# Kernel tuning notes

Measured on AMD Instinct MI355X. Metric: run time of the kernel, lower is better.

The kernel has to match this reference:

```python
import jax, jax.numpy as jnp
import numpy as np

BATCH, SEQ, IN, HID, OUT = 128, 1024, 256, 512, 256


def setup_inputs() -> dict:
    key = jax.random.key(0)
    k_x, k_wi, k_bi, k_wo, k_bo = jax.random.split(key, 5)
    # torch.nn.Linear default init: U(-1/sqrt(fan_in), 1/sqrt(fan_in))
    s_i = 1.0 / np.sqrt(IN + HID)
    s_o = 1.0 / np.sqrt(HID)
    return {
        "x": jax.random.normal(k_x, (BATCH, SEQ, IN), dtype=jnp.float32),
        "W_i2h": jax.random.uniform(k_wi, (HID, IN + HID), jnp.float32, -s_i, s_i),
        "b_i2h": jax.random.uniform(k_bi, (HID,), jnp.float32, -s_i, s_i),
        "W_h2o": jax.random.uniform(k_wo, (OUT, HID), jnp.float32, -s_o, s_o),
        "b_h2o": jax.random.uniform(k_bo, (OUT,), jnp.float32, -s_o, s_o),
    }


def reference(x, W_i2h, b_i2h, W_h2o, b_h2o):
    batch = x.shape[0]
    hid = W_i2h.shape[0]
    # Split i2h weight into input and hidden blocks: cat(x_t, h) @ W.T == x_t @ Wx.T + h @ Wh.T
    Wx = W_i2h[:, : x.shape[-1]]  # (hid, in)
    Wh = W_i2h[:, x.shape[-1] :]  # (hid, hid)
    # Precompute input contributions for all timesteps in one GEMM: (B,S,hid)
    xW = jnp.einsum("bsi,hi->bsh", x, Wx) + b_i2h

    def step(h, xw_t):
        h_new = jnp.tanh(xw_t + h @ Wh.T)
        return h_new, h_new

    h0 = jnp.zeros((batch, hid), dtype=x.dtype)
    h_last, hs = jax.lax.scan(step, h0, jnp.swapaxes(xW, 0, 1))  # hs: (S,B,hid)
    hs = jnp.swapaxes(hs, 0, 1)  # (B,S,hid)
    outputs = jnp.einsum("bsh,oh->bso", hs, W_h2o) + b_h2o  # (B,S,out)
    return outputs, h_last
```

## Files before the change

### kernel.cpp

```cpp
#include <hip/hip_runtime.h>

typedef __attribute__((ext_vector_type(8))) short bf16frag;
typedef __attribute__((ext_vector_type(4))) float f32x4;

constexpr int B = 128, S = 1024, DI = 256, DH = 512, DO = 256;
constexpr int NBUF = 4;
constexpr size_t OUT_MAIN = (size_t)B * S * DO;
constexpr size_t HBUF_BYTES = (size_t)NBUF * B * DH * 2;
constexpr size_t FLAGS_BYTES = 8 * 64 * 4;
constexpr int WH_OFF = 0;
constexpr int WX_OFF = 16384;
constexpr int WHO_OFF = 24576;
constexpr int LDS_BYTES = 65536;

__device__ __forceinline__ void release_vm() {
  asm volatile("s_waitcnt vmcnt(0)" ::: "memory");
}
__device__ __forceinline__ void acquire_cc() {
  asm volatile("" ::: "memory");
}

__device__ __forceinline__ unsigned short f2bf(float f) {
  unsigned int u = __float_as_uint(f);
  u += 0x7fffu + ((u >> 16) & 1u);
  return (unsigned short)(u >> 16);
}
__device__ __forceinline__ float bf2f(unsigned short h) {
  return __uint_as_float(((unsigned int)h) << 16);
}
__device__ __forceinline__ float fast_tanh(float x) {
  float e = __expf(2.0f * x);
  return 1.0f - 2.0f * __builtin_amdgcn_rcpf(e + 1.0f);
}
__device__ __forceinline__ bf16frag cvt8(float4 a, float4 b) {
  bf16frag r;
  r[0]=(short)f2bf(a.x); r[1]=(short)f2bf(a.y); r[2]=(short)f2bf(a.z); r[3]=(short)f2bf(a.w);
  r[4]=(short)f2bf(b.x); r[5]=(short)f2bf(b.y); r[6]=(short)f2bf(b.z); r[7]=(short)f2bf(b.w);
  return r;
}
__device__ __forceinline__ bf16frag load8(const void* base, size_t off, bool fp32m) {
  if (fp32m) {
    const float4* p = reinterpret_cast<const float4*>((const float*)base + off);
    return cvt8(p[0], p[1]);
  }
  return *reinterpret_cast<const bf16frag*>((const unsigned short*)base + off);
}

__device__ __forceinline__ void cluster_wait(const int* f01, const int* f2, int T1, int T2) {
  const int lane = threadIdx.x & 63;
  const int* addr;
  int thr;
  if (lane < 32)      { addr = f01 + lane;        thr = T1; }
  else if (lane < 48) { addr = f2 + (lane - 32);  thr = T2; }
  else                { addr = f01;               thr = (int)0x80000000; }
  int guard = 0;
  while (true) {
    int v = __hip_atomic_load(addr, __ATOMIC_RELAXED, __HIP_MEMORY_SCOPE_AGENT);
    if (__all(v >= thr)) break;
    if (++guard > (1 << 26)) break;
    __builtin_amdgcn_s_sleep(1);
  }
}

__global__ void __launch_bounds__(192, 1)
rnn_persistent(const void* __restrict__ xv,
               const void* __restrict__ Wi2hv,
               const void* __restrict__ biv,
               const void* __restrict__ Whov,
               const void* __restrict__ bov,
               void* __restrict__ outv,
               unsigned short* __restrict__ hbuf,
               int* __restrict__ flags) {
  extern __shared__ unsigned short lds[];
  const int tid = threadIdx.x;
  const int lane = tid & 63;
  const int wave = tid >> 6;
  const int blk = blockIdx.x;
  const int c   = blk & 7;
  const int mem = blk >> 3;
  const int b0  = c * 16;
  const int n_base = mem * 32;
  const int o_base = mem * 16;

  bool fp32m;
  {
    const unsigned short* xu = (const unsigned short*)xv;
    int c0 = 0;
    for (int i = lane; i < 4096; i += 64)
      c0 += (((xu[i] >> 7) & 0xFF) >= 0xC0);
    #pragma unroll
    for (int s = 32; s; s >>= 1) c0 += __shfl_xor(c0, s, 64);
    fp32m = (c0 > 100);
  }

  for (int i = tid; i < 32 * 64; i += 192) {
    int r = i >> 6, bk = i & 63;
    bf16frag v = load8(Wi2hv, (size_t)(n_base + r) * 768 + 256 + bk * 8, fp32m);
    *reinterpret_cast<bf16frag*>(lds + WH_OFF + r * 512 + ((bk ^ (r & 7)) * 8)) = v;
  }
  for (int i = tid; i < 32 * 32; i += 192) {
    int r = i >> 5, bk = i & 31;
    bf16frag v = load8(Wi2hv, (size_t)(n_base + r) * 768 + bk * 8, fp32m);
    *reinterpret_cast<bf16frag*>(lds + WX_OFF + r * 256 + ((bk ^ (r & 7)) * 8)) = v;
  }
  for (int i = tid; i < 16 * 64; i += 192) {
    int r = i >> 6, bk = i & 63;
    bf16frag v = load8(Whov, (size_t)(o_base + r) * 512 + bk * 8, fp32m);
    *reinterpret_cast<bf16frag*>(lds + WHO_OFF + r * 512 + ((bk ^ (r & 7)) * 8)) = v;
  }
  __syncthreads();

  int* f01 = flags + c * 64;
  int* f2  = f01 + 32;
  const int q  = lane >> 4;
  const int ln = lane & 15;
  float* outf = (float*)outv;
  unsigned short* outh = (unsigned short*)outv;

  if (wave < 2) {
    const int nlB  = wave * 16 + ln;
    const int n_g  = n_base + nlB;
    const float bias = fp32m ? ((const float*)biv)[n_g]
                             : bf2f(((const unsigned short*)biv)[n_g]);
    const int swz = nlB & 7;
    const size_t xrow = (size_t)(b0 + ln) * (S * DI) + q * 8;
    const int flag_idx = mem * 2 + wave;
    const size_t hrow_off = (size_t)(b0 + ln) * DH + q * 8;

    bf16frag xf[8];
    #pragma unroll
    for (int cc = 0; cc < 8; ++cc)
      xf[cc] = load8(xv, xrow + cc * 32, fp32m);

    for (int t = 0; t < S; ++t) {
      f32x4 acc = {bias, bias, bias, bias};
      #pragma unroll
      for (int cc = 0; cc < 8; ++cc) {
        bf16frag wf = *reinterpret_cast<const bf16frag*>(
            lds + WX_OFF + nlB * 256 + (((cc * 4 + q) ^ swz) * 8));
        acc = __builtin_amdgcn_mfma_f32_16x16x32_bf16(xf[cc], wf, acc, 0, 0, 0);
      }
      if (t + 1 < S) {
        #pragma unroll
        for (int cc = 0; cc < 8; ++cc)
          xf[cc] = load8(xv, xrow + (size_t)(t + 1) * DI + cc * 32, fp32m);
      }
      if (t > 0) {
        cluster_wait(f01, f2, t, t - 3);
        acquire_cc();
        const unsigned short* hsrc = hbuf + (size_t)((t - 1) & 3) * (B * DH) + hrow_off;
        unsigned long long hlo[16], hhi[16];
        #pragma unroll
        for (int cc = 0; cc < 16; ++cc) {
          const unsigned long long* p = reinterpret_cast<const unsigned long long*>(hsrc + cc * 32);
          hlo[cc] = __hip_atomic_load(p,     __ATOMIC_RELAXED, __HIP_MEMORY_SCOPE_AGENT);
          hhi[cc] = __hip_atomic_load(p + 1, __ATOMIC_RELAXED, __HIP_MEMORY_SCOPE_AGENT);
        }
        #pragma unroll
        for (int cc = 0; cc < 16; ++cc) {
          union { unsigned long long u[2]; bf16frag f; } cvt;
          cvt.u[0] = hlo[cc]; cvt.u[1] = hhi[cc];
          bf16frag wf = *reinterpret_cast<const bf16frag*>(
              lds + WH_OFF + nlB * 512 + (((cc * 4 + q) ^ swz) * 8));
          acc = __builtin_amdgcn_mfma_f32_16x16x32_bf16(cvt.f, wf, acc, 0, 0, 0);
        }
      }
      unsigned short* hdst = hbuf + (size_t)(t & 3) * (B * DH);
      #pragma unroll
      for (int r = 0; r < 4; ++r) {
        float hv = fast_tanh(acc[r]);
        unsigned short hu = f2bf(hv);
        unsigned int other = __shfl_xor((unsigned int)hu, 1, 64);
        if ((lane & 1) == 0) {
          unsigned int packed = (unsigned int)hu | (other << 16);
          __hip_atomic_store(reinterpret_cast<unsigned int*>(
              hdst + (size_t)(b0 + q * 4 + r) * DH + n_g),
              packed, __ATOMIC_RELAXED, __HIP_MEMORY_SCOPE_AGENT);
        }
        if (t == S - 1) {
          size_t hidx = OUT_MAIN + (size_t)(b0 + q * 4 + r) * DH + n_g;
          if (fp32m) outf[hidx] = hv; else outh[hidx] = hu;
        }
      }
      release_vm();
      if (lane == 0)
        __hip_atomic_store(f01 + flag_idx, t + 1, __ATOMIC_RELAXED, __HIP_MEMORY_SCOPE_AGENT);
    }
  } else {
    const int o_g = o_base + ln;
    const float bias = fp32m ? ((const float*)bov)[o_g]
                             : bf2f(((const unsigned short*)bov)[o_g]);
    const int swz = ln & 7;
    const size_t hrow_off = (size_t)(b0 + ln) * DH + q * 8;
    for (int u = 0; u < S; ++u) {
      cluster_wait(f01, f2, u + 1, (int)0x80000000);
      acquire_cc();
      const unsigned short* hsrc = hbuf + (size_t)(u & 3) * (B * DH) + hrow_off;
      unsigned long long hlo[16], hhi[16];
      #pragma unroll
      for (int cc = 0; cc < 16; ++cc) {
        const unsigned long long* p = reinterpret_cast<const unsigned long long*>(hsrc + cc * 32);
        hlo[cc] = __hip_atomic_load(p,     __ATOMIC_RELAXED, __HIP_MEMORY_SCOPE_AGENT);
        hhi[cc] = __hip_atomic_load(p + 1, __ATOMIC_RELAXED, __HIP_MEMORY_SCOPE_AGENT);
      }
      f32x4 acc = {bias, bias, bias, bias};
      #pragma unroll
      for (int cc = 0; cc < 16; ++cc) {
        union { unsigned long long u[2]; bf16frag f; } cvt;
        cvt.u[0] = hlo[cc]; cvt.u[1] = hhi[cc];
        bf16frag wf = *reinterpret_cast<const bf16frag*>(
            lds + WHO_OFF + ln * 512 + (((cc * 4 + q) ^ swz) * 8));
        acc = __builtin_amdgcn_mfma_f32_16x16x32_bf16(cvt.f, wf, acc, 0, 0, 0);
      }
      #pragma unroll
      for (int r = 0; r < 4; ++r) {
        size_t oidx = ((size_t)(b0 + q * 4 + r) * S + u) * DO + o_g;
        if (fp32m) outf[oidx] = acc[r]; else outh[oidx] = f2bf(acc[r]);
      }
      release_vm();
      if (lane == 0)
        __hip_atomic_store(f2 + mem, u + 1, __ATOMIC_RELAXED, __HIP_MEMORY_SCOPE_AGENT);
    }
  }
}

extern "C" void kernel_launch(void* const* d_in, const int* in_sizes, int n_in,
                              void* d_out, int out_size, void* d_ws, size_t ws_size,
                              hipStream_t stream) {
  const void* x    = d_in[0];
  const void* Wi2h = d_in[1];
  const void* bi   = d_in[2];
  const void* Who  = d_in[3];
  const void* bo   = d_in[4];
  void* out = d_out;
  unsigned short* hbuf = (unsigned short*)d_ws;
  int* flags = (int*)((char*)d_ws + HBUF_BYTES);
  if (ws_size < HBUF_BYTES + FLAGS_BYTES) return;

  hipMemsetAsync(flags, 0, FLAGS_BYTES, stream);

  void* args[] = { (void*)&x, (void*)&Wi2h, (void*)&bi, (void*)&Who, (void*)&bo,
                   (void*)&out, (void*)&hbuf, (void*)&flags };
  hipError_t e = hipLaunchCooperativeKernel((void*)rnn_persistent, dim3(128), dim3(192),
                                            args, LDS_BYTES, stream);
  if (e != hipSuccess) {
    rnn_persistent<<<dim3(128), dim3(192), LDS_BYTES, stream>>>(
        x, Wi2h, bi, Who, bo, out, hbuf, flags);
  }
}
```

Before: 8.605 ms.

## Replace per-block flag polling with per-slot atomic counters and deeper h ring buffer

Each wave used to poll 48 per-block flags with a wave-wide vote. Now it waits on two per-slot atomic counters that producers increment with fetch_add, so the wait reads only two addresses. The h ring buffer grows from 4 to up to 16 slots, sized to the workspace, which lets the output-projection waves lag further behind the recurrence before they stall it. The cost is contended atomic increments on a shared counter from 32 or 16 blocks per step, plus more workspace memory.

Measured after the change: 8.835 ms. 2.7% more time.

```diff
diff --git a/kernel.cpp b/kernel.cpp
--- a/kernel.cpp
+++ b/kernel.cpp
@@ -4,10 +4,10 @@
 typedef __attribute__((ext_vector_type(4))) float f32x4;
 
 constexpr int B = 128, S = 1024, DI = 256, DH = 512, DO = 256;
-constexpr int NBUF = 4;
+constexpr int MAXNB = 16;
 constexpr size_t OUT_MAIN = (size_t)B * S * DO;
-constexpr size_t HBUF_BYTES = (size_t)NBUF * B * DH * 2;
-constexpr size_t FLAGS_BYTES = 8 * 64 * 4;
+constexpr size_t SLOT_BYTES = (size_t)B * DH * 2;
+constexpr size_t FLAGS_BYTES = 8 * 2 * MAXNB * 64;
 constexpr int WH_OFF = 0;
 constexpr int WX_OFF = 16384;
 constexpr int WHO_OFF = 24576;
@@ -46,17 +46,12 @@
   return *reinterpret_cast<const bf16frag*>((const unsigned short*)base + off);
 }
 
-__device__ __forceinline__ void cluster_wait(const int* f01, const int* f2, int T1, int T2) {
-  const int lane = threadIdx.x & 63;
-  const int* addr;
-  int thr;
-  if (lane < 32)      { addr = f01 + lane;        thr = T1; }
-  else if (lane < 48) { addr = f2 + (lane - 32);  thr = T2; }
-  else                { addr = f01;               thr = (int)0x80000000; }
+__device__ __forceinline__ void wait2(const int* a1, int t1, const int* a2, int t2) {
   int guard = 0;
   while (true) {
-    int v = __hip_atomic_load(addr, __ATOMIC_RELAXED, __HIP_MEMORY_SCOPE_AGENT);
-    if (__all(v >= thr)) break;
+    int v1 = __hip_atomic_load(a1, __ATOMIC_RELAXED, __HIP_MEMORY_SCOPE_AGENT);
+    int v2 = __hip_atomic_load(a2, __ATOMIC_RELAXED, __HIP_MEMORY_SCOPE_AGENT);
+    if (v1 >= t1 && v2 >= t2) break;
     if (++guard > (1 << 26)) break;
     __builtin_amdgcn_s_sleep(1);
   }
@@ -70,7 +65,8 @@
                const void* __restrict__ bov,
                void* __restrict__ outv,
                unsigned short* __restrict__ hbuf,
-               int* __restrict__ flags) {
+               int* __restrict__ flags,
+               int nm, int lg) {
   extern __shared__ unsigned short lds[];
   const int tid = threadIdx.x;
   const int lane = tid & 63;
@@ -110,8 +106,7 @@
   }
   __syncthreads();
 
-  int* f01 = flags + c * 64;
-  int* f2  = f01 + 32;
+  int* cnt = flags + c * (2 * MAXNB * 16);
   const int q  = lane >> 4;
   const int ln = lane & 15;
   float* outf = (float*)outv;
@@ -124,7 +119,6 @@
                              : bf2f(((const unsigned short*)biv)[n_g]);
     const int swz = nlB & 7;
     const size_t xrow = (size_t)(b0 + ln) * (S * DI) + q * 8;
-    const int flag_idx = mem * 2 + wave;
     const size_t hrow_off = (size_t)(b0 + ln) * DH + q * 8;
 
     bf16frag xf[8];
@@ -146,9 +140,14 @@
           xf[cc] = load8(xv, xrow + (size_t)(t + 1) * DI + cc * 32, fp32m);
       }
       if (t > 0) {
-        cluster_wait(f01, f2, t, t - 3);
+        const int* a1 = cnt + ((t - 1) & nm) * 16;
+        int th1 = 32 * (((t - 1) >> lg) + 1);
+        const int* a2 = a1;
+        int th2 = th1;
+        if (t > nm) { a2 = cnt + (MAXNB + (t & nm)) * 16; th2 = 16 * (t >> lg); }
+        wait2(a1, th1, a2, th2);
         acquire_cc();
-        const unsigned short* hsrc = hbuf + (size_t)((t - 1) & 3) * (B * DH) + hrow_off;
+        const unsigned short* hsrc = hbuf + (size_t)((t - 1) & nm) * (B * DH) + hrow_off;
         unsigned long long hlo[16], hhi[16];
         #pragma unroll
         for (int cc = 0; cc < 16; ++cc) {
@@ -165,7 +164,7 @@
           acc = __builtin_amdgcn_mfma_f32_16x16x32_bf16(cvt.f, wf, acc, 0, 0, 0);
         }
       }
-      unsigned short* hdst = hbuf + (size_t)(t & 3) * (B * DH);
+      unsigned short* hdst = hbuf + (size_t)(t & nm) * (B * DH);
       #pragma unroll
       for (int r = 0; r < 4; ++r) {
         float hv = fast_tanh(acc[r]);
@@ -184,7 +183,8 @@
       }
       release_vm();
       if (lane == 0)
-        __hip_atomic_store(f01 + flag_idx, t + 1, __ATOMIC_RELAXED, __HIP_MEMORY_SCOPE_AGENT);
+        __hip_atomic_fetch_add(cnt + (t & nm) * 16, 1,
+                               __ATOMIC_RELAXED, __HIP_MEMORY_SCOPE_AGENT);
     }
   } else {
     const int o_g = o_base + ln;
@@ -193,9 +193,11 @@
     const int swz = ln & 7;
     const size_t hrow_off = (size_t)(b0 + ln) * DH + q * 8;
     for (int u = 0; u < S; ++u) {
-      cluster_wait(f01, f2, u + 1, (int)0x80000000);
+      const int* a1 = cnt + (u & nm) * 16;
+      int th1 = 32 * ((u >> lg) + 1);
+      wait2(a1, th1, a1, th1);
       acquire_cc();
-      const unsigned short* hsrc = hbuf + (size_t)(u & 3) * (B * DH) + hrow_off;
+      const unsigned short* hsrc = hbuf + (size_t)(u & nm) * (B * DH) + hrow_off;
       unsigned long long hlo[16], hhi[16];
       #pragma unroll
       for (int cc = 0; cc < 16; ++cc) {
@@ -219,7 +221,8 @@
       }
       release_vm();
       if (lane == 0)
-        __hip_atomic_store(f2 + mem, u + 1, __ATOMIC_RELAXED, __HIP_MEMORY_SCOPE_AGENT);
+        __hip_atomic_fetch_add(cnt + (MAXNB + (u & nm)) * 16, 1,
+                               __ATOMIC_RELAXED, __HIP_MEMORY_SCOPE_AGENT);
     }
   }
 }
@@ -233,18 +236,24 @@
   const void* Who  = d_in[3];
   const void* bo   = d_in[4];
   void* out = d_out;
+
+  int nb = MAXNB;
+  while ((size_t)nb * SLOT_BYTES + FLAGS_BYTES > ws_size && nb > 4) nb >>= 1;
+  if ((size_t)nb * SLOT_BYTES + FLAGS_BYTES > ws_size) return;
+  int nm = nb - 1;
+  int lg = (nb == 16) ? 4 : (nb == 8) ? 3 : 2;
+
   unsigned short* hbuf = (unsigned short*)d_ws;
-  int* flags = (int*)((char*)d_ws + HBUF_BYTES);
-  if (ws_size < HBUF_BYTES + FLAGS_BYTES) return;
+  int* flags = (int*)((char*)d_ws + (size_t)nb * SLOT_BYTES);
 
   hipMemsetAsync(flags, 0, FLAGS_BYTES, stream);
 
   void* args[] = { (void*)&x, (void*)&Wi2h, (void*)&bi, (void*)&Who, (void*)&bo,
-                   (void*)&out, (void*)&hbuf, (void*)&flags };
+                   (void*)&out, (void*)&hbuf, (void*)&flags, (void*)&nm, (void*)&lg };
   hipError_t e = hipLaunchCooperativeKernel((void*)rnn_persistent, dim3(128), dim3(192),
                                             args, LDS_BYTES, stream);
   if (e != hipSuccess) {
     rnn_persistent<<<dim3(128), dim3(192), LDS_BYTES, stream>>>(
-        x, Wi2h, bi, Who, bo, out, hbuf, flags);
-  }
-}
+        x, Wi2h, bi, Who, bo, out, hbuf, flags, nm, lg);
+  }
+}
```
